# Performance work log

Measured on AMD Instinct MI355X. Metric: run time of the kernel, lower is better.

## Reference

```python
import jax, jax.numpy as jnp
import numpy as np

S, B, H, K = 4096, 1, 2048, 2  # seq_len, batch (forced to 1 by the view()), hidden_dim, conv kernel
EMBED = K * K                  # embed_dim must equal kernel_size**2
THRESHOLD = 0.0


def setup_inputs() -> dict:
    key = jax.random.key(0)
    k0, k1, k2 = jax.random.split(key, 3)
    inputs = jax.random.normal(k0, (S, B, EMBED), dtype=jnp.float32)
    # ConvFilter params: Conv2d(1,1,K) on a KxK patch == dot with flattened kernel + bias
    conv_w = jax.random.normal(k1, (EMBED,), dtype=jnp.float32) * 0.5
    conv_b = jnp.zeros((1,), dtype=jnp.float32)
    # Four gate Linears (1+H -> H) stacked column-wise into one (1+H, 4H) matmul
    # order: forget | input | update | output  (same math as 4 separate nn.Linear)
    w_gates = (jax.random.normal(k2, (1 + H, 4 * H), dtype=jnp.float32)
               / np.sqrt(1.0 + H)).astype(jnp.float32)
    b_gates = jnp.zeros((4 * H,), dtype=jnp.float32)
    return {"inputs": inputs, "conv_w": conv_w, "conv_b": conv_b,
            "w_gates": w_gates, "b_gates": b_gates}


def reference(inputs, conv_w, conv_b, w_gates, b_gates):
    S_, B_, _ = inputs.shape
    H_ = w_gates.shape[1] // 4

    # Conv preprocess (vectorized over all timesteps): each (K,K) token patch
    # -> scalar sigmoid(conv(x) - threshold), then mean over the per-step batch
    # (batch==1, so the mean is the value itself, matching torch's .mean()).
    conv_scalar = jax.nn.sigmoid(inputs @ conv_w + conv_b[0] - THRESHOLD)  # (S, B)
    conv_scalar = jnp.mean(conv_scalar, axis=1, keepdims=True)             # (S, 1)
    conv_out = jnp.broadcast_to(conv_scalar[:, :, None], (S_, B_, 1))      # (S, B, 1)

    hx0 = jnp.zeros((B_, H_), dtype=inputs.dtype)
    cx0 = jnp.zeros((B_, H_), dtype=inputs.dtype)

    def step(carry, c_t):
        hx, cx = carry
        combined = jnp.concatenate([c_t, hx], axis=1)        # (B, 1+H)
        gates = combined @ w_gates + b_gates                  # (B, 4H) fused 4-gate GEMM
        f, i, g, o = jnp.split(gates, 4, axis=1)
        f = jax.nn.sigmoid(f)
        i = jax.nn.sigmoid(i)
        g = jnp.tanh(g)
        o = jax.nn.sigmoid(o)
        cx = f * cx + i * g
        hx = o * jnp.tanh(cx)
        return (hx, cx), hx

    (hx, cx), stacked = jax.lax.scan(step, (hx0, cx0), conv_out)
    return stacked, hx, cx
```

## Files before the change

kernel.cpp:

```cpp
#include <hip/hip_runtime.h>
#include <math.h>

#define S_LEN 4096
#define HID   2048
#define NBLK  256
#define NTHR  512

typedef unsigned long long u64;


__global__ __launch_bounds__(NTHR, 2)
void qlstm_persistent(const float* __restrict__ inp,
                      const float* __restrict__ conv_w,
                      const float* __restrict__ conv_b,
                      const float* __restrict__ Wg,
                      const float* __restrict__ bg,
                      float* __restrict__ out,
                      float* __restrict__ ws)
{
    const int b   = blockIdx.x;
    const int tid = threadIdx.x;
    const int l   = tid & 63;
    const int wv  = tid >> 6;

    u64* tb0 = (u64*)ws;
    u64* tb1 = tb0 + HID + 16;

    __shared__ __align__(16) float hx_lds[HID];
    __shared__ __align__(16) float conv_lds[S_LEN];
    __shared__ float gates_lds[32];
    __shared__ float colw0[32];
    __shared__ float colb[32];

    {
        const float cw0 = conv_w[0], cw1 = conv_w[1], cw2 = conv_w[2], cw3 = conv_w[3];
        const float cb  = conv_b[0];
        for (int g = tid; g < S_LEN; g += NTHR) {
            float4 x = ((const float4*)inp)[g];
            float v = x.x*cw0 + x.y*cw1 + x.z*cw2 + x.w*cw3 + cb;
            conv_lds[g] = 1.0f / (1.0f + expf(-v));
        }
    }

    int jcol[4];
    #pragma unroll
    for (int c = 0; c < 4; ++c) {
        int cgi  = 4*wv + c;
        int gate = cgi >> 3;
        int mi   = cgi & 7;
        jcol[c]  = (gate << 11) + (b * 8 + mi);
    }
    if (l == 0) {
        #pragma unroll
        for (int c = 0; c < 4; ++c) {
            int cgi = 4*wv + c;
            colw0[cgi] = Wg[jcol[c]];
            colb[cgi]  = bg[jcol[c]];
        }
    }

    float wreg[4][32];
    #pragma unroll
    for (int j = 0; j < 8; ++j)
        #pragma unroll
        for (int r = 0; r < 4; ++r) {
            const float* rowp = Wg + (size_t)(1 + 4*l + 256*j + r) * 8192;
            #pragma unroll
            for (int c = 0; c < 4; ++c)
                wreg[c][4*j + r] = rowp[jcol[c]];
        }

    float cx = 0.0f;
    const int m_out = b * 8 + tid;

    if (tid < 8)
        __hip_atomic_store(&tb0[m_out], (u64)1 << 32,
                           __ATOMIC_RELAXED, __HIP_MEMORY_SCOPE_AGENT);

    const int ebase = (wv << 8) + l;

    for (int t = 0; t < S_LEN; ++t) {
        const unsigned want = (unsigned)(t + 1);
        u64* tb = (t & 1) ? tb1 : tb0;
        u64* tn = (t & 1) ? tb0 : tb1;

        u64 v0 = 0, v1 = 0, v2 = 0, v3 = 0;
        unsigned pend = 0xFu;
        do {
            if (pend & 1u) v0 = __hip_atomic_load(&tb[ebase      ], __ATOMIC_RELAXED, __HIP_MEMORY_SCOPE_AGENT);
            if (pend & 2u) v1 = __hip_atomic_load(&tb[ebase +  64], __ATOMIC_RELAXED, __HIP_MEMORY_SCOPE_AGENT);
            if (pend & 4u) v2 = __hip_atomic_load(&tb[ebase + 128], __ATOMIC_RELAXED, __HIP_MEMORY_SCOPE_AGENT);
            if (pend & 8u) v3 = __hip_atomic_load(&tb[ebase + 192], __ATOMIC_RELAXED, __HIP_MEMORY_SCOPE_AGENT);
            if ((unsigned)(v0 >> 32) == want) pend &= ~1u;
            if ((unsigned)(v1 >> 32) == want) pend &= ~2u;
            if ((unsigned)(v2 >> 32) == want) pend &= ~4u;
            if ((unsigned)(v3 >> 32) == want) pend &= ~8u;
        } while (pend);
        hx_lds[ebase      ] = __uint_as_float((unsigned)v0);
        hx_lds[ebase +  64] = __uint_as_float((unsigned)v1);
        hx_lds[ebase + 128] = __uint_as_float((unsigned)v2);
        hx_lds[ebase + 192] = __uint_as_float((unsigned)v3);
        __syncthreads();

        const float4* hl = (const float4*)hx_lds;
        float acc0 = 0.f, acc1 = 0.f, acc2 = 0.f, acc3 = 0.f;
        #pragma unroll
        for (int j = 0; j < 8; ++j) {
            float4 h = hl[l + 64*j];
            acc0 = fmaf(h.x, wreg[0][4*j+0], acc0);
            acc1 = fmaf(h.x, wreg[1][4*j+0], acc1);
            acc2 = fmaf(h.x, wreg[2][4*j+0], acc2);
            acc3 = fmaf(h.x, wreg[3][4*j+0], acc3);
            acc0 = fmaf(h.y, wreg[0][4*j+1], acc0);
            acc1 = fmaf(h.y, wreg[1][4*j+1], acc1);
            acc2 = fmaf(h.y, wreg[2][4*j+1], acc2);
            acc3 = fmaf(h.y, wreg[3][4*j+1], acc3);
            acc0 = fmaf(h.z, wreg[0][4*j+2], acc0);
            acc1 = fmaf(h.z, wreg[1][4*j+2], acc1);
            acc2 = fmaf(h.z, wreg[2][4*j+2], acc2);
            acc3 = fmaf(h.z, wreg[3][4*j+2], acc3);
            acc0 = fmaf(h.w, wreg[0][4*j+3], acc0);
            acc1 = fmaf(h.w, wreg[1][4*j+3], acc1);
            acc2 = fmaf(h.w, wreg[2][4*j+3], acc2);
            acc3 = fmaf(h.w, wreg[3][4*j+3], acc3);
        }
        #pragma unroll
        for (int off = 32; off; off >>= 1) {
            acc0 += __shfl_down(acc0, off, 64);
            acc1 += __shfl_down(acc1, off, 64);
            acc2 += __shfl_down(acc2, off, 64);
            acc3 += __shfl_down(acc3, off, 64);
        }
        if (l == 0) {
            gates_lds[4*wv + 0] = acc0;
            gates_lds[4*wv + 1] = acc1;
            gates_lds[4*wv + 2] = acc2;
            gates_lds[4*wv + 3] = acc3;
        }
        __syncthreads();

        if (tid < 8) {
            float ct = conv_lds[t];
            float fg = gates_lds[tid]      + ct*colw0[tid]      + colb[tid];
            float ig = gates_lds[8 + tid]  + ct*colw0[8 + tid]  + colb[8 + tid];
            float gg = gates_lds[16 + tid] + ct*colw0[16 + tid] + colb[16 + tid];
            float og = gates_lds[24 + tid] + ct*colw0[24 + tid] + colb[24 + tid];
            float f  = 1.0f / (1.0f + expf(-fg));
            float ii = 1.0f / (1.0f + expf(-ig));
            float gv = tanhf(gg);
            float o  = 1.0f / (1.0f + expf(-og));
            cx = f * cx + ii * gv;
            float hx = o * tanhf(cx);
            __hip_atomic_store(&tn[m_out],
                               ((u64)(unsigned)(t + 2) << 32) | (u64)__float_as_uint(hx),
                               __ATOMIC_RELAXED, __HIP_MEMORY_SCOPE_AGENT);
            out[(size_t)t * HID + m_out] = hx;
            if (t == S_LEN - 1) {
                out[(size_t)S_LEN * HID + m_out]       = hx;
                out[(size_t)S_LEN * HID + HID + m_out] = cx;
            }
        }
    }
}

extern "C" void kernel_launch(void* const* d_in, const int* in_sizes, int n_in,
                              void* d_out, int out_size, void* d_ws, size_t ws_size,
                              hipStream_t stream) {
    const float* inp    = (const float*)d_in[0];
    const float* conv_w = (const float*)d_in[1];
    const float* conv_b = (const float*)d_in[2];
    const float* Wg     = (const float*)d_in[3];
    const float* bg     = (const float*)d_in[4];
    float* out = (float*)d_out;
    float* ws  = (float*)d_ws;


    void* args[] = {(void*)&inp, (void*)&conv_w, (void*)&conv_b,
                    (void*)&Wg, (void*)&bg, (void*)&out, (void*)&ws};
    hipLaunchCooperativeKernel((void*)qlstm_persistent,
                               dim3(NBLK), dim3(NTHR), args, 0, stream);
}
```

Measured before the change: 11.65 ms.

## Give each wave one hidden unit, double-buffer hx, drop second block barrier

```diff
diff --git a/kernel.cpp b/kernel.cpp
--- a/kernel.cpp
+++ b/kernel.cpp
@@ -7,7 +7,17 @@
 #define NTHR  512
 
 typedef unsigned long long u64;
+typedef float v2f __attribute__((ext_vector_type(2)));
 
+
+__device__ __forceinline__ float fsig(float x) {
+    return 1.0f / (1.0f + __expf(-x));
+}
+__device__ __forceinline__ float ftanh(float x) {
+    float e = __expf(2.0f * fabsf(x));
+    float r = 1.0f - 2.0f / (e + 1.0f);
+    return copysignf(r, x);
+}
 
 __global__ __launch_bounds__(NTHR, 2)
 void qlstm_persistent(const float* __restrict__ inp,
@@ -26,11 +36,8 @@
     u64* tb0 = (u64*)ws;
     u64* tb1 = tb0 + HID + 16;
 
-    __shared__ __align__(16) float hx_lds[HID];
+    __shared__ __align__(16) float hx_lds[2][HID];
     __shared__ __align__(16) float conv_lds[S_LEN];
-    __shared__ float gates_lds[32];
-    __shared__ float colw0[32];
-    __shared__ float colb[32];
 
     {
         const float cw0 = conv_w[0], cw1 = conv_w[1], cw2 = conv_w[2], cw3 = conv_w[3];
@@ -38,51 +45,46 @@
         for (int g = tid; g < S_LEN; g += NTHR) {
             float4 x = ((const float4*)inp)[g];
             float v = x.x*cw0 + x.y*cw1 + x.z*cw2 + x.w*cw3 + cb;
-            conv_lds[g] = 1.0f / (1.0f + expf(-v));
+            conv_lds[g] = fsig(v);
         }
     }
 
+    const int unit = b * 8 + wv;
     int jcol[4];
     #pragma unroll
+    for (int c = 0; c < 4; ++c) jcol[c] = (c << 11) + unit;
+
+    float cw_r[4], cb_r[4];
+    #pragma unroll
     for (int c = 0; c < 4; ++c) {
-        int cgi  = 4*wv + c;
-        int gate = cgi >> 3;
-        int mi   = cgi & 7;
-        jcol[c]  = (gate << 11) + (b * 8 + mi);
-    }
-    if (l == 0) {
-        #pragma unroll
-        for (int c = 0; c < 4; ++c) {
-            int cgi = 4*wv + c;
-            colw0[cgi] = Wg[jcol[c]];
-            colb[cgi]  = bg[jcol[c]];
-        }
+        cw_r[c] = Wg[jcol[c]];
+        cb_r[c] = bg[jcol[c]];
     }
 
-    float wreg[4][32];
+    v2f wreg2[4][16];
     #pragma unroll
     for (int j = 0; j < 8; ++j)
         #pragma unroll
-        for (int r = 0; r < 4; ++r) {
-            const float* rowp = Wg + (size_t)(1 + 4*l + 256*j + r) * 8192;
+        for (int p = 0; p < 2; ++p) {
+            const float* r0 = Wg + (size_t)(1 + 4*l + 256*j + 2*p) * 8192;
+            const float* r1 = r0 + 8192;
             #pragma unroll
             for (int c = 0; c < 4; ++c)
-                wreg[c][4*j + r] = rowp[jcol[c]];
+                wreg2[c][2*j + p] = (v2f){ r0[jcol[c]], r1[jcol[c]] };
         }
 
     float cx = 0.0f;
-    const int m_out = b * 8 + tid;
+    const int ebase = (wv << 8) + l;
 
     if (tid < 8)
-        __hip_atomic_store(&tb0[m_out], (u64)1 << 32,
+        __hip_atomic_store(&tb0[b * 8 + tid], (u64)1 << 32,
                            __ATOMIC_RELAXED, __HIP_MEMORY_SCOPE_AGENT);
-
-    const int ebase = (wv << 8) + l;
 
     for (int t = 0; t < S_LEN; ++t) {
         const unsigned want = (unsigned)(t + 1);
         u64* tb = (t & 1) ? tb1 : tb0;
         u64* tn = (t & 1) ? tb0 : tb1;
+        float* hbuf = hx_lds[t & 1];
 
         u64 v0 = 0, v1 = 0, v2 = 0, v3 = 0;
         unsigned pend = 0xFu;
@@ -96,34 +98,32 @@
             if ((unsigned)(v2 >> 32) == want) pend &= ~4u;
             if ((unsigned)(v3 >> 32) == want) pend &= ~8u;
         } while (pend);
-        hx_lds[ebase      ] = __uint_as_float((unsigned)v0);
-        hx_lds[ebase +  64] = __uint_as_float((unsigned)v1);
-        hx_lds[ebase + 128] = __uint_as_float((unsigned)v2);
-        hx_lds[ebase + 192] = __uint_as_float((unsigned)v3);
+        hbuf[ebase      ] = __uint_as_float((unsigned)v0);
+        hbuf[ebase +  64] = __uint_as_float((unsigned)v1);
+        hbuf[ebase + 128] = __uint_as_float((unsigned)v2);
+        hbuf[ebase + 192] = __uint_as_float((unsigned)v3);
         __syncthreads();
 
-        const float4* hl = (const float4*)hx_lds;
-        float acc0 = 0.f, acc1 = 0.f, acc2 = 0.f, acc3 = 0.f;
+        const float4* hl = (const float4*)hbuf;
+        v2f a0 = {0.f, 0.f}, a1 = {0.f, 0.f}, a2 = {0.f, 0.f}, a3 = {0.f, 0.f};
         #pragma unroll
         for (int j = 0; j < 8; ++j) {
             float4 h = hl[l + 64*j];
-            acc0 = fmaf(h.x, wreg[0][4*j+0], acc0);
-            acc1 = fmaf(h.x, wreg[1][4*j+0], acc1);
-            acc2 = fmaf(h.x, wreg[2][4*j+0], acc2);
-            acc3 = fmaf(h.x, wreg[3][4*j+0], acc3);
-            acc0 = fmaf(h.y, wreg[0][4*j+1], acc0);
-            acc1 = fmaf(h.y, wreg[1][4*j+1], acc1);
-            acc2 = fmaf(h.y, wreg[2][4*j+1], acc2);
-            acc3 = fmaf(h.y, wreg[3][4*j+1], acc3);
-            acc0 = fmaf(h.z, wreg[0][4*j+2], acc0);
-            acc1 = fmaf(h.z, wreg[1][4*j+2], acc1);
-            acc2 = fmaf(h.z, wreg[2][4*j+2], acc2);
-            acc3 = fmaf(h.z, wreg[3][4*j+2], acc3);
-            acc0 = fmaf(h.w, wreg[0][4*j+3], acc0);
-            acc1 = fmaf(h.w, wreg[1][4*j+3], acc1);
-            acc2 = fmaf(h.w, wreg[2][4*j+3], acc2);
-            acc3 = fmaf(h.w, wreg[3][4*j+3], acc3);
+            v2f h01 = { h.x, h.y };
+            v2f h23 = { h.z, h.w };
+            a0 = __builtin_elementwise_fma(h01, wreg2[0][2*j  ], a0);
+            a1 = __builtin_elementwise_fma(h01, wreg2[1][2*j  ], a1);
+            a2 = __builtin_elementwise_fma(h01, wreg2[2][2*j  ], a2);
+            a3 = __builtin_elementwise_fma(h01, wreg2[3][2*j  ], a3);
+            a0 = __builtin_elementwise_fma(h23, wreg2[0][2*j+1], a0);
+            a1 = __builtin_elementwise_fma(h23, wreg2[1][2*j+1], a1);
+            a2 = __builtin_elementwise_fma(h23, wreg2[2][2*j+1], a2);
+            a3 = __builtin_elementwise_fma(h23, wreg2[3][2*j+1], a3);
         }
+        float acc0 = a0.x + a0.y;
+        float acc1 = a1.x + a1.y;
+        float acc2 = a2.x + a2.y;
+        float acc3 = a3.x + a3.y;
         #pragma unroll
         for (int off = 32; off; off >>= 1) {
             acc0 += __shfl_down(acc0, off, 64);
@@ -131,33 +131,22 @@
             acc2 += __shfl_down(acc2, off, 64);
             acc3 += __shfl_down(acc3, off, 64);
         }
+
         if (l == 0) {
-            gates_lds[4*wv + 0] = acc0;
-            gates_lds[4*wv + 1] = acc1;
-            gates_lds[4*wv + 2] = acc2;
-            gates_lds[4*wv + 3] = acc3;
-        }
-        __syncthreads();
-
-        if (tid < 8) {
             float ct = conv_lds[t];
-            float fg = gates_lds[tid]      + ct*colw0[tid]      + colb[tid];
-            float ig = gates_lds[8 + tid]  + ct*colw0[8 + tid]  + colb[8 + tid];
-            float gg = gates_lds[16 + tid] + ct*colw0[16 + tid] + colb[16 + tid];
-            float og = gates_lds[24 + tid] + ct*colw0[24 + tid] + colb[24 + tid];
-            float f  = 1.0f / (1.0f + expf(-fg));
-            float ii = 1.0f / (1.0f + expf(-ig));
-            float gv = tanhf(gg);
-            float o  = 1.0f / (1.0f + expf(-og));
+            float f  = fsig (acc0 + ct*cw_r[0] + cb_r[0]);
+            float ii = fsig (acc1 + ct*cw_r[1] + cb_r[1]);
+            float gv = ftanh(acc2 + ct*cw_r[2] + cb_r[2]);
+            float o  = fsig (acc3 + ct*cw_r[3] + cb_r[3]);
             cx = f * cx + ii * gv;
-            float hx = o * tanhf(cx);
-            __hip_atomic_store(&tn[m_out],
+            float hx = o * ftanh(cx);
+            __hip_atomic_store(&tn[unit],
                                ((u64)(unsigned)(t + 2) << 32) | (u64)__float_as_uint(hx),
                                __ATOMIC_RELAXED, __HIP_MEMORY_SCOPE_AGENT);
-            out[(size_t)t * HID + m_out] = hx;
+            out[(size_t)t * HID + unit] = hx;
             if (t == S_LEN - 1) {
-                out[(size_t)S_LEN * HID + m_out]       = hx;
-                out[(size_t)S_LEN * HID + HID + m_out] = cx;
+                out[(size_t)S_LEN * HID + unit]       = hx;
+                out[(size_t)S_LEN * HID + HID + unit] = cx;
             }
         }
     }
```

After: 19.17 ms. +64.5%, slower.
